# Performance work log

Hardware: AMD Instinct MI355X
Metric: run time of the kernel (lower is better)

## Reference

```python
import jax, jax.numpy as jnp
import numpy as np

B, N, FDIM, REL, H = 4, 256, 256, 16, 8
D = FDIM // H


def setup_inputs() -> dict:
    key = jax.random.key(0)
    ks = jax.random.split(key, 10)
    s_f = 1.0 / np.sqrt(FDIM)
    s_kv = 1.0 / np.sqrt(FDIM + REL)
    return {
        "node_features": jax.random.normal(ks[0], (B, N, FDIM), jnp.float32),
        "relative_positions": jax.random.normal(ks[1], (B, N, N, REL), jnp.float32),
        # torch Linear weights stored transposed -> here [in, out]
        "Wq": jax.random.uniform(ks[2], (FDIM, FDIM), jnp.float32, -s_f, s_f),
        "bq": jax.random.uniform(ks[3], (FDIM,), jnp.float32, -s_f, s_f),
        "Wk": jax.random.uniform(ks[4], (FDIM + REL, FDIM), jnp.float32, -s_kv, s_kv),
        "bk": jax.random.uniform(ks[5], (FDIM,), jnp.float32, -s_kv, s_kv),
        "Wv": jax.random.uniform(ks[6], (FDIM + REL, FDIM), jnp.float32, -s_kv, s_kv),
        "bv": jax.random.uniform(ks[7], (FDIM,), jnp.float32, -s_kv, s_kv),
        "Wo": jax.random.uniform(ks[8], (FDIM, FDIM), jnp.float32, -s_f, s_f),
        "bo": jax.random.uniform(ks[9], (FDIM,), jnp.float32, -s_f, s_f),
    }


def reference(node_features, relative_positions, Wq, bq, Wk, bk, Wv, bv, Wo, bo):
    b, n, f = node_features.shape
    # Q: [b, n_i, H, D]
    Q = (node_features @ Wq + bq).reshape(b, n, H, D)
    # per-edge K/V input: [b, i, j, f+rel] where feature part is node j's features
    nf_j = jnp.broadcast_to(node_features[:, None, :, :], (b, n, n, f))
    kv_in = jnp.concatenate([nf_j, relative_positions], axis=-1)
    K = (kv_in @ Wk + bk).reshape(b, n, n, H, D)  # [b, i, j, h, d]
    V = (kv_in @ Wv + bv).reshape(b, n, n, H, D)
    scale = 1.0 / jnp.sqrt(jnp.asarray(D, node_features.dtype))
    scores = jnp.einsum('bihd,bijhd->bhij', Q, K) * scale
    attn = jax.nn.softmax(scores, axis=-1)
    wv = jnp.einsum('bhij,bijhd->bihd', attn, V).reshape(b, n, f)
    return node_features + (wv @ Wo + bo)
```

## Files before the change

### kernel.cpp

```cpp
#include <hip/hip_runtime.h>


#define BB 4
#define NN 256
#define FD 256
#define RL 16
#define NH 8
#define HD 32

#define OFF_Q    0
#define OFF_KN   (BB*NN*FD)
#define OFF_VN   (OFF_KN + BB*NN*FD/2)
#define OFF_WO   (OFF_VN + BB*NN*FD/2)

#define ATP 260
#define RLT 130

static __device__ __forceinline__ unsigned short f2bf(float x) {
  unsigned int u = __float_as_uint(x);
  unsigned int r = (u + 0x7fffu + ((u >> 16) & 1u)) >> 16;
  return (unsigned short)r;
}
static __device__ __forceinline__ float bf2f(unsigned short h) {
  return __uint_as_float(((unsigned int)h) << 16);
}

__global__ __launch_bounds__(256, 4) void k_qkv9(
    const float* __restrict__ nf,
    const float* __restrict__ Wq, const float* __restrict__ bq,
    const float* __restrict__ Wk, const float* __restrict__ bk,
    const float* __restrict__ Wv, const float* __restrict__ bv,
    const float* __restrict__ Wo,
    float* __restrict__ ws) {
  const int tid = threadIdx.x;
  const int sel = blockIdx.y;
  if (sel == 3) {
    if (blockIdx.x < 128) {
      const int k2 = blockIdx.x;
      unsigned int lo = f2bf(Wo[(2 * k2) * FD + tid]);
      unsigned int hi = f2bf(Wo[(2 * k2 + 1) * FD + tid]);
      ((unsigned int*)(ws + OFF_WO))[k2 * FD + tid] = lo | (hi << 16);
    }
    return;
  }
  const int ROWS = 4;
  __shared__ float lrowT[FD][ROWS];
  const int row0 = blockIdx.x * ROWS;
  const float* W; const float* bias;
  if (sel == 0)      { W = Wq; bias = bq; }
  else if (sel == 1) { W = Wk; bias = bk; }
  else               { W = Wv; bias = bv; }
  #pragma unroll
  for (int t = 0; t < ROWS; ++t)
    lrowT[tid][t] = nf[(row0 + t) * FD + tid];
  __syncthreads();
  float acc[ROWS] = {0.f, 0.f, 0.f, 0.f};
  #pragma unroll 16
  for (int k = 0; k < FD; ++k) {
    const float w = W[k * FD + tid];
    float4 a0 = *(const float4*)&lrowT[k][0];
    acc[0] += a0.x * w; acc[1] += a0.y * w; acc[2] += a0.z * w; acc[3] += a0.w * w;
  }
  const float bb = bias[tid];
  if (sel == 1) {
    const int b2 = row0 >> 8, i0 = row0 & 255;
    unsigned short* kout = (unsigned short*)(ws + OFF_KN) + ((size_t)b2 * FD + tid) * NN + i0;
    ushort4 v0;
    v0.x = f2bf(acc[0] + bb); v0.y = f2bf(acc[1] + bb);
    v0.z = f2bf(acc[2] + bb); v0.w = f2bf(acc[3] + bb);
    *((ushort4*)kout) = v0;
  } else if (sel == 2) {
    unsigned short* outp = (unsigned short*)(ws + OFF_VN);
    #pragma unroll
    for (int r = 0; r < ROWS; ++r)
      outp[(size_t)(row0 + r) * FD + tid] = f2bf(acc[r] + bb);
  } else {
    float* outp = ws + OFF_Q;
    #pragma unroll
    for (int r = 0; r < ROWS; ++r)
      outp[(row0 + r) * FD + tid] = acc[r] + bb;
  }
}

__global__ __launch_bounds__(256, 4) void k_attn9(
    const float* __restrict__ rel,
    const float* __restrict__ Wk,
    const float* __restrict__ Wv,
    const float* __restrict__ nf,
    const float* __restrict__ bo,
    float* __restrict__ out,
    float* __restrict__ ws) {
  const float* Q = ws + OFF_Q;
  const unsigned short* KnB = (const unsigned short*)(ws + OFF_KN);
  const unsigned short* VnB = (const unsigned short*)(ws + OFF_VN);
  const unsigned int* WoP = (const unsigned int*)(ws + OFF_WO);

  const int bid = (blockIdx.x & 7) * 64 + (blockIdx.x >> 3);
  const int b  = bid >> 7;
  const int i0 = (bid & 127) * 2;
  const int tid = threadIdx.x;
  const int l = tid & 63, w = tid >> 6;

  __shared__ float q[2][FD];
  __shared__ float qrs[2][NH * RL];
  __shared__ float ar[2][NH * RL];
  __shared__ __align__(16) float at[2 * NH * ATP];
  __shared__ __align__(16) unsigned int rldsT[2 * RL * RLT];
  float* part = (float*)rldsT;
  float* wvT  = (float*)rldsT + 2048;

  const float scale = 0.17677669529663687f;
  q[0][tid] = Q[(b * NN + i0) * FD + tid] * scale;
  q[1][tid] = Q[(b * NN + i0 + 1) * FD + tid] * scale;

  #pragma unroll
  for (int ii = 0; ii < 2; ++ii) {
    const float4* rp = (const float4*)(rel + ((size_t)(b * NN + i0 + ii)) * (NN * RL));
    #pragma unroll
    for (int m = 0; m < 2; ++m) {
      const int t = tid + 256 * m;
      const int jp = t >> 2, q4 = t & 3;
      float4 va = rp[8 * jp + q4];
      float4 vb = rp[8 * jp + 4 + q4];
      unsigned int* base = &rldsT[(ii * RL + 4 * q4) * RLT + jp];
      base[0]       = (unsigned int)f2bf(va.x) | ((unsigned int)f2bf(vb.x) << 16);
      base[RLT]     = (unsigned int)f2bf(va.y) | ((unsigned int)f2bf(vb.y) << 16);
      base[2 * RLT] = (unsigned int)f2bf(va.z) | ((unsigned int)f2bf(vb.z) << 16);
      base[3 * RLT] = (unsigned int)f2bf(va.w) | ((unsigned int)f2bf(vb.w) << 16);
    }
  }

  {
    const int ii = l >> 5, hh = (l >> 4) & 1, r = l & 15;
    const int h = 2 * w + hh;
    const float* wrow = Wk + (FD + r) * FD + h * HD;
    const float* qq = &q[ii][h * HD];
    float a = 0.f;
    #pragma unroll
    for (int d = 0; d < HD; ++d) a += qq[d] * wrow[d];
    qrs[ii][h * RL + r] = a;
  }
  __syncthreads();

  float s[2][2][4];
  #pragma unroll
  for (int ii = 0; ii < 2; ++ii)
    #pragma unroll
    for (int hh = 0; hh < 2; ++hh)
      #pragma unroll
      for (int jj = 0; jj < 4; ++jj) s[ii][hh][jj] = 0.f;
  {
    const ushort4* kp = (const ushort4*)(KnB + ((size_t)b * FD + 64 * w) * NN) + l;
    #pragma unroll 2
    for (int dd = 0; dd < 8; ++dd) {
      float4 qv00 = *(const float4*)&q[0][64 * w + 4 * dd];
      float4 qv01 = *(const float4*)&q[0][64 * w + 32 + 4 * dd];
      float4 qv10 = *(const float4*)&q[1][64 * w + 4 * dd];
      float4 qv11 = *(const float4*)&q[1][64 * w + 32 + 4 * dd];
      #pragma unroll
      for (int e = 0; e < 4; ++e) {
        ushort4 u0 = kp[(4 * dd + e) * (NN / 4)];
        ushort4 u1 = kp[(32 + 4 * dd + e) * (NN / 4)];
        float4 k0 = make_float4(bf2f(u0.x), bf2f(u0.y), bf2f(u0.z), bf2f(u0.w));
        float4 k1 = make_float4(bf2f(u1.x), bf2f(u1.y), bf2f(u1.z), bf2f(u1.w));
        const float a0 = (&qv00.x)[e], a1 = (&qv01.x)[e];
        const float b0 = (&qv10.x)[e], b1 = (&qv11.x)[e];
        s[0][0][0] += a0 * k0.x; s[0][0][1] += a0 * k0.y;
        s[0][0][2] += a0 * k0.z; s[0][0][3] += a0 * k0.w;
        s[1][0][0] += b0 * k0.x; s[1][0][1] += b0 * k0.y;
        s[1][0][2] += b0 * k0.z; s[1][0][3] += b0 * k0.w;
        s[0][1][0] += a1 * k1.x; s[0][1][1] += a1 * k1.y;
        s[0][1][2] += a1 * k1.z; s[0][1][3] += a1 * k1.w;
        s[1][1][0] += b1 * k1.x; s[1][1][1] += b1 * k1.y;
        s[1][1][2] += b1 * k1.z; s[1][1][3] += b1 * k1.w;
      }
    }
  }

  #pragma unroll
  for (int ii = 0; ii < 2; ++ii) {
    #pragma unroll
    for (int r = 0; r < RL; ++r) {
      uint2 u = *(const uint2*)&rldsT[(ii * RL + r) * RLT + 2 * l];
      float r0 = bf2f((unsigned short)(u.x & 0xffffu));
      float r1 = bf2f((unsigned short)(u.x >> 16));
      float r2 = bf2f((unsigned short)(u.y & 0xffffu));
      float r3 = bf2f((unsigned short)(u.y >> 16));
      const float qa = qrs[ii][(2 * w) * RL + r];
      const float qb = qrs[ii][(2 * w + 1) * RL + r];
      s[ii][0][0] += qa * r0; s[ii][0][1] += qa * r1;
      s[ii][0][2] += qa * r2; s[ii][0][3] += qa * r3;
      s[ii][1][0] += qb * r0; s[ii][1][1] += qb * r1;
      s[ii][1][2] += qb * r2; s[ii][1][3] += qb * r3;
    }
  }

  #pragma unroll
  for (int ii = 0; ii < 2; ++ii) {
    #pragma unroll
    for (int hh = 0; hh < 2; ++hh) {
      float v = fmaxf(fmaxf(s[ii][hh][0], s[ii][hh][1]),
                      fmaxf(s[ii][hh][2], s[ii][hh][3]));
      #pragma unroll
      for (int off = 32; off; off >>= 1) v = fmaxf(v, __shfl_xor(v, off));
      float4 p;
      p.x = __expf(s[ii][hh][0] - v); p.y = __expf(s[ii][hh][1] - v);
      p.z = __expf(s[ii][hh][2] - v); p.w = __expf(s[ii][hh][3] - v);
      float sum = p.x + p.y + p.z + p.w;
      #pragma unroll
      for (int off = 32; off; off >>= 1) sum += __shfl_xor(sum, off);
      const float rec = 1.f / sum;
      p.x *= rec; p.y *= rec; p.z *= rec; p.w *= rec;
      *(float4*)&at[(ii * NH + 2 * w + hh) * ATP + 4 * l] = p;
    }
  }

  #pragma unroll
  for (int ii = 0; ii < 2; ++ii) {
    const int r = l & 15, sl = l >> 4;
    const int h = 2 * w + (sl & 1);
    const int jb = (sl >> 1) * 128;
    const float* atp = at + (ii * NH + h) * ATP + jb;
    const unsigned int* rr_ = &rldsT[(ii * RL + r) * RLT + (jb >> 1)];
    float a = 0.f;
    #pragma unroll 8
    for (int u = 0; u < 64; ++u) {
      unsigned int x = rr_[u];
      a += atp[2 * u]     * bf2f((unsigned short)(x & 0xffffu));
      a += atp[2 * u + 1] * bf2f((unsigned short)(x >> 16));
    }
    a += __shfl_xor(a, 32);
    if (l < 32) ar[ii][32 * w + l] = a;
  }
  __syncthreads();

  {
    const int h = l >> 3;
    const ushort4* vp = (const ushort4*)(VnB + (size_t)b * NN * FD) + l;
    const float* ap0 = at + h * ATP + 64 * w;
    const float* ap1 = at + (NH + h) * ATP + 64 * w;
    float4 a0 = make_float4(0,0,0,0), a1 = make_float4(0,0,0,0);
    #pragma unroll 4
    for (int jj = 0; jj < 64; ++jj) {
      ushort4 u = vp[(64 * w + jj) * (FD / 4)];
      float4 v = make_float4(bf2f(u.x), bf2f(u.y), bf2f(u.z), bf2f(u.w));
      float p0 = ap0[jj], p1 = ap1[jj];
      a0.x += p0*v.x; a0.y += p0*v.y; a0.z += p0*v.z; a0.w += p0*v.w;
      a1.x += p1*v.x; a1.y += p1*v.y; a1.z += p1*v.z; a1.w += p1*v.w;
    }
    ((float4*)part)[w * 64 + l]       = a0;
    ((float4*)part)[(4 + w) * 64 + l] = a1;
  }
  __syncthreads();

  {
    const int c = tid, h2 = c >> 5;
    float s0 = part[c] + part[FD + c] + part[2*FD + c] + part[3*FD + c];
    float s1 = part[4*FD + c] + part[5*FD + c] + part[6*FD + c] + part[7*FD + c];
    #pragma unroll
    for (int r = 0; r < RL; ++r) {
      const float wvr = Wv[(FD + r) * FD + c];
      s0 += ar[0][h2 * RL + r] * wvr;
      s1 += ar[1][h2 * RL + r] * wvr;
    }
    *(float2*)&wvT[2 * c] = make_float2(s0, s1);
  }
  __syncthreads();

  {
    const int c = tid;
    float acc0 = 0.f, acc1 = 0.f;
    #pragma unroll 8
    for (int k2 = 0; k2 < 128; ++k2) {
      unsigned int u = WoP[k2 * FD + c];
      float w0 = bf2f((unsigned short)(u & 0xffffu));
      float w1 = bf2f((unsigned short)(u >> 16));
      float2 wa = *(const float2*)&wvT[4 * k2];
      float2 wb = *(const float2*)&wvT[4 * k2 + 2];
      acc0 += wa.x * w0 + wb.x * w1;
      acc1 += wa.y * w0 + wb.y * w1;
    }
    const float bb = bo[c];
    const int row = b * NN + i0;
    out[row * FD + c]       = nf[row * FD + c]       + acc0 + bb;
    out[(row + 1) * FD + c] = nf[(row + 1) * FD + c] + acc1 + bb;
  }
}

extern "C" void kernel_launch(void* const* d_in, const int* in_sizes, int n_in,
                              void* d_out, int out_size, void* d_ws, size_t ws_size,
                              hipStream_t stream) {
  const float* nf  = (const float*)d_in[0];
  const float* rel = (const float*)d_in[1];
  const float* Wq  = (const float*)d_in[2];
  const float* bq  = (const float*)d_in[3];
  const float* Wk  = (const float*)d_in[4];
  const float* bk  = (const float*)d_in[5];
  const float* Wv  = (const float*)d_in[6];
  const float* bv  = (const float*)d_in[7];
  const float* Wo  = (const float*)d_in[8];
  const float* bo  = (const float*)d_in[9];
  float* out = (float*)d_out;
  float* ws  = (float*)d_ws;

  k_qkv9 <<<dim3(BB * NN / 4, 4), 256, 0, stream>>>(nf, Wq, bq, Wk, bk, Wv, bv, Wo, ws);
  k_attn9<<<BB * NN / 2, 256, 0, stream>>>(rel, Wk, Wv, nf, bo, out, ws);
}
```

Before: 43.40 us.

## Move Q/K/V and output projections to bf16 MFMA kernels

Replaces the scalar FP32 Q/K/V projection and the per-block Wo projection with separate bf16 MFMA (16x16x32) GEMM kernels. A prep kernel converts node features and transposes the weights into bf16. The attention kernel now writes its bf16 output to workspace, and a new output kernel applies Wo, the bias and the residual. This lowers the FMA cost of the projections, but it adds two kernel launches, extra workspace round trips and more bf16 rounding.

```diff
diff --git a/kernel.cpp b/kernel.cpp
--- a/kernel.cpp
+++ b/kernel.cpp
@@ -8,10 +8,15 @@
 #define NH 8
 #define HD 32
 
+typedef __attribute__((ext_vector_type(8))) short bf16x8;
+typedef __attribute__((ext_vector_type(4))) float f32x4;
+
 #define OFF_Q    0
 #define OFF_KN   (BB*NN*FD)
 #define OFF_VN   (OFF_KN + BB*NN*FD/2)
-#define OFF_WO   (OFF_VN + BB*NN*FD/2)
+#define OFF_WVB  (OFF_VN + BB*NN*FD/2)
+#define OFF_NFB  (OFF_WVB + BB*NN*FD/2)
+#define OFF_WT   (OFF_NFB + BB*NN*FD/2)
 
 #define ATP 260
 #define RLT 130
@@ -25,75 +30,106 @@
   return __uint_as_float(((unsigned int)h) << 16);
 }
 
-__global__ __launch_bounds__(256, 4) void k_qkv9(
+__global__ __launch_bounds__(256) void k_prep(
     const float* __restrict__ nf,
-    const float* __restrict__ Wq, const float* __restrict__ bq,
-    const float* __restrict__ Wk, const float* __restrict__ bk,
-    const float* __restrict__ Wv, const float* __restrict__ bv,
-    const float* __restrict__ Wo,
+    const float* __restrict__ Wq, const float* __restrict__ Wk,
+    const float* __restrict__ Wv, const float* __restrict__ Wo,
     float* __restrict__ ws) {
   const int tid = threadIdx.x;
   const int sel = blockIdx.y;
-  if (sel == 3) {
-    if (blockIdx.x < 128) {
-      const int k2 = blockIdx.x;
-      unsigned int lo = f2bf(Wo[(2 * k2) * FD + tid]);
-      unsigned int hi = f2bf(Wo[(2 * k2 + 1) * FD + tid]);
-      ((unsigned int*)(ws + OFF_WO))[k2 * FD + tid] = lo | (hi << 16);
+  if (sel == 4) {
+    unsigned short* nfB = (unsigned short*)(ws + OFF_NFB);
+    const int base = blockIdx.x * 16384;
+    #pragma unroll 8
+    for (int k = 0; k < 64; ++k) {
+      const int idx = base + k * 256 + tid;
+      nfB[idx] = f2bf(nf[idx]);
     }
     return;
   }
-  const int ROWS = 4;
-  __shared__ float lrowT[FD][ROWS];
-  const int row0 = blockIdx.x * ROWS;
-  const float* W; const float* bias;
-  if (sel == 0)      { W = Wq; bias = bq; }
-  else if (sel == 1) { W = Wk; bias = bk; }
-  else               { W = Wv; bias = bv; }
-  #pragma unroll
-  for (int t = 0; t < ROWS; ++t)
-    lrowT[tid][t] = nf[(row0 + t) * FD + tid];
+  const float* W = (sel == 0) ? Wq : (sel == 1) ? Wk : (sel == 2) ? Wv : Wo;
+  unsigned short* WT = (unsigned short*)(ws + OFF_WT) + sel * FD * FD;
+  __shared__ unsigned short t[64][72];
+  const int tx = blockIdx.x & 3, ty = blockIdx.x >> 2;
+  const int cx = tid & 63, r0 = tid >> 6;
+  #pragma unroll
+  for (int rr = r0; rr < 64; rr += 4)
+    t[rr][cx] = f2bf(W[(ty * 64 + rr) * FD + tx * 64 + cx]);
   __syncthreads();
-  float acc[ROWS] = {0.f, 0.f, 0.f, 0.f};
-  #pragma unroll 16
-  for (int k = 0; k < FD; ++k) {
-    const float w = W[k * FD + tid];
-    float4 a0 = *(const float4*)&lrowT[k][0];
-    acc[0] += a0.x * w; acc[1] += a0.y * w; acc[2] += a0.z * w; acc[3] += a0.w * w;
-  }
-  const float bb = bias[tid];
-  if (sel == 1) {
-    const int b2 = row0 >> 8, i0 = row0 & 255;
-    unsigned short* kout = (unsigned short*)(ws + OFF_KN) + ((size_t)b2 * FD + tid) * NN + i0;
-    ushort4 v0;
-    v0.x = f2bf(acc[0] + bb); v0.y = f2bf(acc[1] + bb);
-    v0.z = f2bf(acc[2] + bb); v0.w = f2bf(acc[3] + bb);
-    *((ushort4*)kout) = v0;
-  } else if (sel == 2) {
-    unsigned short* outp = (unsigned short*)(ws + OFF_VN);
-    #pragma unroll
-    for (int r = 0; r < ROWS; ++r)
-      outp[(size_t)(row0 + r) * FD + tid] = f2bf(acc[r] + bb);
+  #pragma unroll
+  for (int rr = r0; rr < 64; rr += 4)
+    WT[(tx * 64 + rr) * FD + ty * 64 + cx] = t[cx][rr];
+}
+
+__global__ __launch_bounds__(256) void k_proj(
+    const float* __restrict__ bq, const float* __restrict__ bk,
+    const float* __restrict__ bv, float* __restrict__ ws) {
+  const unsigned short* nfB = (const unsigned short*)(ws + OFF_NFB);
+  const int mat = blockIdx.y >> 2;
+  const int c0 = (blockIdx.y & 3) * 64;
+  const int m0 = blockIdx.x * 64 + (threadIdx.x >> 6) * 16;
+  const int l = threadIdx.x & 63;
+  const unsigned short* WT = (const unsigned short*)(ws + OFF_WT) + mat * FD * FD;
+  const int ar = l & 15, kg = l >> 4;
+  f32x4 acc[4];
+  #pragma unroll
+  for (int nt = 0; nt < 4; ++nt) acc[nt] = (f32x4){0.f, 0.f, 0.f, 0.f};
+  #pragma unroll
+  for (int ks = 0; ks < 8; ++ks) {
+    bf16x8 a = *(const bf16x8*)(nfB + (m0 + ar) * FD + ks * 32 + kg * 8);
+    #pragma unroll
+    for (int nt = 0; nt < 4; ++nt) {
+      bf16x8 b = *(const bf16x8*)(WT + (c0 + nt * 16 + ar) * FD + ks * 32 + kg * 8);
+      acc[nt] = __builtin_amdgcn_mfma_f32_16x16x32_bf16(a, b, acc[nt], 0, 0, 0);
+    }
+  }
+  if (mat == 0) {
+    const float scale = 0.17677669529663687f;
+    float* Qo = ws + OFF_Q;
+    #pragma unroll
+    for (int nt = 0; nt < 4; ++nt) {
+      const int cc = c0 + nt * 16 + ar;
+      const float bb = bq[cc];
+      #pragma unroll
+      for (int i = 0; i < 4; ++i)
+        Qo[(m0 + kg * 4 + i) * FD + cc] = (acc[nt][i] + bb) * scale;
+    }
+  } else if (mat == 1) {
+    unsigned short* KnT = (unsigned short*)(ws + OFF_KN);
+    const int b2 = m0 >> 8, j0 = (m0 & 255) + kg * 4;
+    #pragma unroll
+    for (int nt = 0; nt < 4; ++nt) {
+      const int cc = c0 + nt * 16 + ar;
+      const float bb = bk[cc];
+      ushort4 v;
+      v.x = f2bf(acc[nt][0] + bb); v.y = f2bf(acc[nt][1] + bb);
+      v.z = f2bf(acc[nt][2] + bb); v.w = f2bf(acc[nt][3] + bb);
+      *(ushort4*)&KnT[((size_t)b2 * FD + cc) * NN + j0] = v;
+    }
   } else {
-    float* outp = ws + OFF_Q;
-    #pragma unroll
-    for (int r = 0; r < ROWS; ++r)
-      outp[(row0 + r) * FD + tid] = acc[r] + bb;
-  }
-}
-
-__global__ __launch_bounds__(256, 4) void k_attn9(
+    unsigned short* Vn = (unsigned short*)(ws + OFF_VN);
+    const int b2 = m0 >> 8;
+    #pragma unroll
+    for (int nt = 0; nt < 4; ++nt) {
+      const int cc = c0 + nt * 16 + ar;
+      const float bb = bv[cc];
+      #pragma unroll
+      for (int i = 0; i < 4; ++i) {
+        const int j = (m0 & 255) + kg * 4 + i;
+        Vn[((size_t)b2 * NN + j) * FD + cc] = f2bf(acc[nt][i] + bb);
+      }
+    }
+  }
+}
+
+__global__ __launch_bounds__(256, 4) void k_attn10(
     const float* __restrict__ rel,
     const float* __restrict__ Wk,
     const float* __restrict__ Wv,
-    const float* __restrict__ nf,
-    const float* __restrict__ bo,
-    float* __restrict__ out,
     float* __restrict__ ws) {
   const float* Q = ws + OFF_Q;
   const unsigned short* KnB = (const unsigned short*)(ws + OFF_KN);
   const unsigned short* VnB = (const unsigned short*)(ws + OFF_VN);
-  const unsigned int* WoP = (const unsigned int*)(ws + OFF_WO);
 
   const int bid = (blockIdx.x & 7) * 64 + (blockIdx.x >> 3);
   const int b  = bid >> 7;
@@ -107,11 +143,9 @@
   __shared__ __align__(16) float at[2 * NH * ATP];
   __shared__ __align__(16) unsigned int rldsT[2 * RL * RLT];
   float* part = (float*)rldsT;
-  float* wvT  = (float*)rldsT + 2048;
-
-  const float scale = 0.17677669529663687f;
-  q[0][tid] = Q[(b * NN + i0) * FD + tid] * scale;
-  q[1][tid] = Q[(b * NN + i0 + 1) * FD + tid] * scale;
+
+  q[0][tid] = Q[(b * NN + i0) * FD + tid];
+  q[1][tid] = Q[(b * NN + i0 + 1) * FD + tid];
 
   #pragma unroll
   for (int ii = 0; ii < 2; ++ii) {
@@ -263,27 +297,42 @@
       s0 += ar[0][h2 * RL + r] * wvr;
       s1 += ar[1][h2 * RL + r] * wvr;
     }
-    *(float2*)&wvT[2 * c] = make_float2(s0, s1);
-  }
-  __syncthreads();
-
-  {
-    const int c = tid;
-    float acc0 = 0.f, acc1 = 0.f;
-    #pragma unroll 8
-    for (int k2 = 0; k2 < 128; ++k2) {
-      unsigned int u = WoP[k2 * FD + c];
-      float w0 = bf2f((unsigned short)(u & 0xffffu));
-      float w1 = bf2f((unsigned short)(u >> 16));
-      float2 wa = *(const float2*)&wvT[4 * k2];
-      float2 wb = *(const float2*)&wvT[4 * k2 + 2];
-      acc0 += wa.x * w0 + wb.x * w1;
-      acc1 += wa.y * w0 + wb.y * w1;
-    }
-    const float bb = bo[c];
-    const int row = b * NN + i0;
-    out[row * FD + c]       = nf[row * FD + c]       + acc0 + bb;
-    out[(row + 1) * FD + c] = nf[(row + 1) * FD + c] + acc1 + bb;
+    unsigned short* wvB = (unsigned short*)(ws + OFF_WVB);
+    wvB[(b * NN + i0) * FD + c]     = f2bf(s0);
+    wvB[(b * NN + i0 + 1) * FD + c] = f2bf(s1);
+  }
+}
+
+__global__ __launch_bounds__(256) void k_out10(
+    const float* __restrict__ nf, const float* __restrict__ bo,
+    float* __restrict__ out, float* __restrict__ ws) {
+  const unsigned short* wvB = (const unsigned short*)(ws + OFF_WVB);
+  const unsigned short* WoT = (const unsigned short*)(ws + OFF_WT) + 3 * FD * FD;
+  const int c0 = blockIdx.y * 64;
+  const int m0 = blockIdx.x * 64 + (threadIdx.x >> 6) * 16;
+  const int l = threadIdx.x & 63;
+  const int ar = l & 15, kg = l >> 4;
+  f32x4 acc[4];
+  #pragma unroll
+  for (int nt = 0; nt < 4; ++nt) acc[nt] = (f32x4){0.f, 0.f, 0.f, 0.f};
+  #pragma unroll
+  for (int ks = 0; ks < 8; ++ks) {
+    bf16x8 a = *(const bf16x8*)(wvB + (m0 + ar) * FD + ks * 32 + kg * 8);
+    #pragma unroll
+    for (int nt = 0; nt < 4; ++nt) {
+      bf16x8 b = *(const bf16x8*)(WoT + (c0 + nt * 16 + ar) * FD + ks * 32 + kg * 8);
+      acc[nt] = __builtin_amdgcn_mfma_f32_16x16x32_bf16(a, b, acc[nt], 0, 0, 0);
+    }
+  }
+  #pragma unroll
+  for (int nt = 0; nt < 4; ++nt) {
+    const int cc = c0 + nt * 16 + ar;
+    const float bb = bo[cc];
+    #pragma unroll
+    for (int i = 0; i < 4; ++i) {
+      const int m = m0 + kg * 4 + i;
+      out[m * FD + cc] = nf[m * FD + cc] + acc[nt][i] + bb;
+    }
   }
 }
 
@@ -303,6 +352,8 @@
   float* out = (float*)d_out;
   float* ws  = (float*)d_ws;
 
-  k_qkv9 <<<dim3(BB * NN / 4, 4), 256, 0, stream>>>(nf, Wq, bq, Wk, bk, Wv, bv, Wo, ws);
-  k_attn9<<<BB * NN / 2, 256, 0, stream>>>(rel, Wk, Wv, nf, bo, out, ws);
-}
+  k_prep  <<<dim3(16, 5), 256, 0, stream>>>(nf, Wq, Wk, Wv, Wo, ws);
+  k_proj  <<<dim3(16, 12), 256, 0, stream>>>(bq, bk, bv, ws);
+  k_attn10<<<512, 256, 0, stream>>>(rel, Wk, Wv, ws);
+  k_out10 <<<dim3(16, 4), 256, 0, stream>>>(nf, bo, out, ws);
+}
```

New measurement: 43.70 us. Within noise of the previous version (+0.7%).
